# Optimization experiments

Measured on AMD Instinct MI355X. Metric: run time of the kernel, lower is better.

## Reference

```python
import jax, jax.numpy as jnp
import numpy as np
from math import sqrt

SIZE = 4096
NR_CORES = 2
RANK = 16
D = 64  # core_size: D**NR_CORES == SIZE


def setup_inputs() -> dict:
    key = jax.random.key(0)
    k_x, k_c0, k_c1, k_b = jax.random.split(key, 4)
    t = 1.0 / sqrt(SIZE)
    sigma = (t * sqrt(RANK) ** (1 - NR_CORES)) ** (1.0 / NR_CORES)
    x = jax.random.normal(k_x, (2, 4096, SIZE), dtype=jnp.float32)
    core0 = sigma * jax.random.normal(k_c0, (D, D, D, RANK, 1), dtype=jnp.float32)
    core1 = sigma * jax.random.normal(k_c1, (D, D, D, 1, RANK), dtype=jnp.float32)
    bias = sqrt(1.0 / SIZE) * jax.random.uniform(k_b, (SIZE,), minval=-1.0, maxval=1.0, dtype=jnp.float32)
    return {"x": x, "core0": core0, "core1": core1, "bias": bias}


def _btt_forward(x, cores, bias):
    d, c, size = D, NR_CORES, SIZE
    G = cores[0]  # (d,...,d, r, 1)
    for idx, core in enumerate(cores[1:]):
        j = d ** (idx + 1)
        i = d ** (c - idx - 1)
        core_r = core.reshape(j, d, i, core.shape[-2], core.shape[-1])
        G_r = G.reshape(j, d ** (idx + 1), i, G.shape[-2], G.shape[-1])
        # contract rank dim b: (j,x,i,cb) x (j,y,i,ba) -> (j,x,y,i,c,a)
        G = jnp.einsum('jxicb,jyiba->jxyica', core_r, G_r)
    G = G.reshape(size, size)
    out = x.reshape(-1, size) @ G + bias
    return out.reshape(x.shape)


def reference(x, core0, core1, bias):
    return _btt_forward(x, [core0, core1], bias)
```

## Files before the change

### kernel.cpp

```cpp
#include <hip/hip_runtime.h>
#include <hip/hip_bf16.h>
#include <stdint.h>
#include <stddef.h>

using bf16 = __hip_bfloat16;

typedef __attribute__((ext_vector_type(4))) float f32x4;
typedef __attribute__((ext_vector_type(8))) short bf16x8;
typedef __attribute__((ext_vector_type(4))) unsigned short u16x4;

#define K_DIM 4096
#define M_ROWS 8192
#define BM 256
#define BN 256
#define BK 64
#define NT (K_DIM / BK)
#define MT2 (M_ROWS / BM)
#define NT2 (K_DIM / BN)

template<int M> struct MC { static constexpr int value = M; };

__global__ void conv_bf16(const float* __restrict__ in, bf16* __restrict__ outb, int n4) {
  int idx = blockIdx.x * blockDim.x + threadIdx.x;
  int stride = gridDim.x * blockDim.x;
  for (int k = idx; k < n4; k += stride) {
    f32x4 v = ((const f32x4*)in)[k];
    bf16 tmp[4];
    tmp[0] = __float2bfloat16(v.x);
    tmp[1] = __float2bfloat16(v.y);
    tmp[2] = __float2bfloat16(v.z);
    tmp[3] = __float2bfloat16(v.w);
    ((u16x4*)outb)[k] = *(const u16x4*)tmp;
  }
}

__global__ void build_gt(const float* __restrict__ core0, const float* __restrict__ core1,
                         bf16* __restrict__ GT) {
  int j = blockIdx.x >> 6;
  int i = blockIdx.x & 63;
  __shared__ float c0s[64][16];
  __shared__ float c1s[64][16];
  int t = threadIdx.x;
#pragma unroll
  for (int rep = 0; rep < 4; ++rep) {
    int idx = rep * 256 + t;
    int row = idx >> 4;
    int b = idx & 15;
    size_t base = ((size_t)(j * 64 + row) * 64 + i) * 16 + b;
    c1s[row][b] = core1[base];
    c0s[row][b] = core0[base];
  }
  __syncthreads();
  int x = t & 63;
  int ys = t >> 6;
  float r1[16];
#pragma unroll
  for (int b = 0; b < 16; ++b) r1[b] = c1s[x][b];
#pragma unroll
  for (int yy = 0; yy < 16; ++yy) {
    int y = ys * 16 + yy;
    float acc = 0.f;
#pragma unroll
    for (int b = 0; b < 16; ++b) acc += r1[b] * c0s[y][b];
    GT[((size_t)(y * 64 + i) << 12) + (size_t)(j * 64 + x)] = __float2bfloat16(acc);
  }
}

__device__ __forceinline__ void gload_lds16(const bf16* g, bf16* l) {
  __builtin_amdgcn_global_load_lds(
      (const __attribute__((address_space(1))) unsigned int*)(g),
      (__attribute__((address_space(3))) unsigned int*)(l),
      16, 0, 0);
}

template<int MH>
__device__ __forceinline__ void read_a(bf16x8 (&af)[4][2], const bf16* As,
                                       int abase, int swk0, int swk1) {
#pragma unroll
  for (int mi = 0; mi < 4; ++mi) {
    int off = abase + (MH * 4 + mi) * 1024;
    af[mi][0] = *(const bf16x8*)&As[off + swk0];
    af[mi][1] = *(const bf16x8*)&As[off + swk1];
  }
}

template<int NH>
__device__ __forceinline__ void read_b(bf16x8 (&bfr)[4][2], const bf16* Bs,
                                       int bbase, int swk0, int swk1) {
#pragma unroll
  for (int ni = 0; ni < 2; ++ni) {
    int off = bbase + (NH * 2 + ni) * 1024;
    bfr[NH * 2 + ni][0] = *(const bf16x8*)&Bs[off + swk0];
    bfr[NH * 2 + ni][1] = *(const bf16x8*)&Bs[off + swk1];
  }
}

template<int MH, int NH>
__device__ __forceinline__ void mfma_quad(f32x4 (&acc)[8][4], const bf16x8 (&af)[4][2],
                                          const bf16x8 (&bfr)[4][2]) {
#pragma unroll
  for (int mi = 0; mi < 4; ++mi)
#pragma unroll
    for (int ni = 0; ni < 2; ++ni)
#pragma unroll
      for (int kk = 0; kk < 2; ++kk)
        acc[MH * 4 + mi][NH * 2 + ni] = __builtin_amdgcn_mfma_f32_16x16x32_bf16(
            af[mi][kk], bfr[NH * 2 + ni][kk], acc[MH * 4 + mi][NH * 2 + ni], 0, 0, 0);
}

#define BARRIER() __builtin_amdgcn_s_barrier()
#define SP1() __builtin_amdgcn_s_setprio(1)
#define SP0() __builtin_amdgcn_s_setprio(0)
#define VMCNT4() asm volatile("s_waitcnt vmcnt(4)" ::: "memory")
#define VMCNT0() asm volatile("s_waitcnt vmcnt(0)" ::: "memory")

__global__ __launch_bounds__(512, 2)
void gemm_xg(const bf16* __restrict__ Xb, const bf16* __restrict__ GT,
             const float* __restrict__ bias, float* __restrict__ out) {
  __shared__ bf16 As[2][BM * BK];
  __shared__ bf16 Bs[2][BN * BK];

  int bid = blockIdx.x;
  int sb = (bid & 7) * (MT2 * NT2 / 8) + (bid >> 3);
  int bm = sb >> 4;
  int bn = sb & 15;

  int t = threadIdx.x;
  int lane = t & 63;
  int wid = t >> 6;

  int srow = t >> 3;
  int scol = t & 7;
  int sxor = scol ^ (srow & 7);
  const bf16* gA0 = Xb + ((size_t)(bm * BM + srow) * K_DIM) + sxor * 8;
  const bf16* gB0 = GT + ((size_t)(bn * BN + srow) * K_DIM) + sxor * 8;
  int lbase = srow * BK + scol * 8;

  auto sA = [&](int buf, int h, int kt) {
    const bf16* g = gA0 + (size_t)(h * 128) * K_DIM + (size_t)kt * BK;
    bf16* l = &As[buf][h * 128 * BK + lbase];
    gload_lds16(g, l);
    gload_lds16(g + (size_t)64 * K_DIM, l + 64 * BK);
  };
  auto sB = [&](int buf, int h, int kt) {
    const bf16* g = gB0 + (size_t)(h * 128) * K_DIM + (size_t)kt * BK;
    bf16* l = &Bs[buf][h * 128 * BK + lbase];
    gload_lds16(g, l);
    gload_lds16(g + (size_t)64 * K_DIM, l + 64 * BK);
  };

  int wm = wid >> 2;
  int wn = wid & 3;
  int lr = lane & 15;
  int g4 = lane >> 4;
  int x7 = lr & 7;
  int swk0 = ((g4 ^ x7) << 3);
  int swk1 = (((4 + g4) ^ x7) << 3);
  int abase = (wm * 128 + lr) * BK;
  int bbase = (wn * 64 + lr) * BK;

  f32x4 acc[8][4] = {};
  bf16x8 af[4][2];
  bf16x8 bfr[4][2];

  auto tile = [&](int kt, const bf16* Ab, const bf16* Bb, int obuf, int cbuf, auto mode) {
    constexpr int MODE = decltype(mode)::value;
    if (MODE == 2) { VMCNT0(); } else { VMCNT4(); }
    BARRIER();
    if (MODE < 2) { sA(obuf, 0, kt + 1); sA(obuf, 1, kt + 1); }
    read_a<0>(af, Ab, abase, swk0, swk1);
    read_b<0>(bfr, Bb, bbase, swk0, swk1);
    read_b<1>(bfr, Bb, bbase, swk0, swk1);
    SP1();
    mfma_quad<0, 0>(acc, af, bfr);
    mfma_quad<0, 1>(acc, af, bfr);
    SP0();
    read_a<1>(af, Ab, abase, swk0, swk1);
    SP1();
    mfma_quad<1, 0>(acc, af, bfr);
    mfma_quad<1, 1>(acc, af, bfr);
    SP0();
    BARRIER();
    if (MODE == 0) { sB(cbuf, 0, kt + 2); sB(cbuf, 1, kt + 2); }
  };

  const bf16* A0 = &As[0][0];
  const bf16* B0 = &Bs[0][0];
  const bf16* A1 = &As[1][0];
  const bf16* B1 = &Bs[1][0];

  sB(0, 0, 0); sB(0, 1, 0);
  sA(0, 0, 0); sA(0, 1, 0);
  sB(1, 0, 1); sB(1, 1, 1);

#pragma unroll 1
  for (int i = 0; i < NT / 2 - 1; ++i) {
    tile(2 * i,     A0, B0, 1, 0, MC<0>{});
    tile(2 * i + 1, A1, B1, 0, 1, MC<0>{});
  }
  tile(NT - 2, A0, B0, 1, 0, MC<1>{});
  tile(NT - 1, A1, B1, 0, 1, MC<2>{});

  int colbase = bn * BN + wn * 64 + lr;
  int rowbase = bm * BM + wm * 128 + g4 * 4;
#pragma unroll
  for (int ni = 0; ni < 4; ++ni) {
    int col = colbase + ni * 16;
    float bv = bias[col];
#pragma unroll
    for (int mi = 0; mi < 8; ++mi) {
#pragma unroll
      for (int r = 0; r < 4; ++r) {
        int row = rowbase + mi * 16 + r;
        out[(size_t)row * K_DIM + col] = acc[mi][ni][r] + bv;
      }
    }
  }
}

extern "C" void kernel_launch(void* const* d_in, const int* in_sizes, int n_in,
                              void* d_out, int out_size, void* d_ws, size_t ws_size,
                              hipStream_t stream) {
  const float* x     = (const float*)d_in[0];
  const float* core0 = (const float*)d_in[1];
  const float* core1 = (const float*)d_in[2];
  const float* bias  = (const float*)d_in[3];
  float* out = (float*)d_out;

  bf16* Xb = (bf16*)d_ws;
  bf16* GT = (bf16*)((char*)d_ws + (size_t)M_ROWS * K_DIM * sizeof(bf16));

  conv_bf16<<<2048, 256, 0, stream>>>(x, Xb, (M_ROWS * K_DIM) / 4);
  build_gt<<<4096, 256, 0, stream>>>(core0, core1, GT);
  gemm_xg<<<MT2 * NT2, 512, 0, stream>>>(Xb, GT, bias, out);
}
```

Before: 297.4 us.

## Restructure GEMM main loop into ping-pong phases overlapping LDS reads with MFMA

The bf16 GEMM main loop becomes a multi-phase schedule. Each tile is split into four barrier-separated phases. The MFMAs for the second M-half of the previous tile are deferred into the next tile's first phase, and partial lgkmcnt waits with sched_barriers let LDS fragment reads and global-to-LDS prefetches overlap compute. The intent is to hide LDS read latency and balance issue across waves. It adds more barriers and more live fragment registers, which may hurt occupancy at 2 blocks per CU or add sync overhead.

```diff
diff --git a/kernel.cpp b/kernel.cpp
--- a/kernel.cpp
+++ b/kernel.cpp
@@ -73,42 +73,15 @@
       16, 0, 0);
 }
 
-template<int MH>
-__device__ __forceinline__ void read_a(bf16x8 (&af)[4][2], const bf16* As,
-                                       int abase, int swk0, int swk1) {
-#pragma unroll
-  for (int mi = 0; mi < 4; ++mi) {
-    int off = abase + (MH * 4 + mi) * 1024;
-    af[mi][0] = *(const bf16x8*)&As[off + swk0];
-    af[mi][1] = *(const bf16x8*)&As[off + swk1];
-  }
-}
-
-template<int NH>
-__device__ __forceinline__ void read_b(bf16x8 (&bfr)[4][2], const bf16* Bs,
-                                       int bbase, int swk0, int swk1) {
-#pragma unroll
-  for (int ni = 0; ni < 2; ++ni) {
-    int off = bbase + (NH * 2 + ni) * 1024;
-    bfr[NH * 2 + ni][0] = *(const bf16x8*)&Bs[off + swk0];
-    bfr[NH * 2 + ni][1] = *(const bf16x8*)&Bs[off + swk1];
-  }
-}
-
-template<int MH, int NH>
-__device__ __forceinline__ void mfma_quad(f32x4 (&acc)[8][4], const bf16x8 (&af)[4][2],
-                                          const bf16x8 (&bfr)[4][2]) {
-#pragma unroll
-  for (int mi = 0; mi < 4; ++mi)
-#pragma unroll
-    for (int ni = 0; ni < 2; ++ni)
-#pragma unroll
-      for (int kk = 0; kk < 2; ++kk)
-        acc[MH * 4 + mi][NH * 2 + ni] = __builtin_amdgcn_mfma_f32_16x16x32_bf16(
-            af[mi][kk], bfr[NH * 2 + ni][kk], acc[MH * 4 + mi][NH * 2 + ni], 0, 0, 0);
-}
-
-#define BARRIER() __builtin_amdgcn_s_barrier()
+#define BARRIER() asm volatile("s_barrier" ::: "memory")
+#define LGKM8F() do { \
+    asm volatile("s_waitcnt lgkmcnt(8)" ::: "memory"); \
+    __builtin_amdgcn_sched_barrier(0); \
+  } while (0)
+#define LGKM0F() do { \
+    asm volatile("s_waitcnt lgkmcnt(0)" ::: "memory"); \
+    __builtin_amdgcn_sched_barrier(0); \
+  } while (0)
 #define SP1() __builtin_amdgcn_s_setprio(1)
 #define SP0() __builtin_amdgcn_s_setprio(0)
 #define VMCNT4() asm volatile("s_waitcnt vmcnt(4)" ::: "memory")
@@ -160,46 +133,106 @@
   int bbase = (wn * 64 + lr) * BK;
 
   f32x4 acc[8][4] = {};
-  bf16x8 af[4][2];
-  bf16x8 bfr[4][2];
-
-  auto tile = [&](int kt, const bf16* Ab, const bf16* Bb, int obuf, int cbuf, auto mode) {
-    constexpr int MODE = decltype(mode)::value;
-    if (MODE == 2) { VMCNT0(); } else { VMCNT4(); }
-    BARRIER();
-    if (MODE < 2) { sA(obuf, 0, kt + 1); sA(obuf, 1, kt + 1); }
-    read_a<0>(af, Ab, abase, swk0, swk1);
-    read_b<0>(bfr, Bb, bbase, swk0, swk1);
-    read_b<1>(bfr, Bb, bbase, swk0, swk1);
-    SP1();
-    mfma_quad<0, 0>(acc, af, bfr);
-    mfma_quad<0, 1>(acc, af, bfr);
-    SP0();
-    read_a<1>(af, Ab, abase, swk0, swk1);
-    SP1();
-    mfma_quad<1, 0>(acc, af, bfr);
-    mfma_quad<1, 1>(acc, af, bfr);
-    SP0();
-    BARRIER();
-    if (MODE == 0) { sB(cbuf, 0, kt + 2); sB(cbuf, 1, kt + 2); }
-  };
-
-  const bf16* A0 = &As[0][0];
-  const bf16* B0 = &Bs[0][0];
-  const bf16* A1 = &As[1][0];
-  const bf16* B1 = &Bs[1][0];
+  bf16x8 a0[4][2], a1[4][2];
+  bf16x8 b0[2][2], b1[2][2];
+
+  auto rdA0 = [&](const bf16* Ab) {
+#pragma unroll
+    for (int mi = 0; mi < 4; ++mi) {
+      int off = abase + mi * 1024;
+      a0[mi][0] = *(const bf16x8*)&Ab[off + swk0];
+      a0[mi][1] = *(const bf16x8*)&Ab[off + swk1];
+    }
+  };
+  auto rdA1 = [&](const bf16* Ab) {
+#pragma unroll
+    for (int mi = 0; mi < 4; ++mi) {
+      int off = abase + (4 + mi) * 1024;
+      a1[mi][0] = *(const bf16x8*)&Ab[off + swk0];
+      a1[mi][1] = *(const bf16x8*)&Ab[off + swk1];
+    }
+  };
+  auto rdB01 = [&](const bf16* Bb) {
+#pragma unroll
+    for (int ni = 0; ni < 2; ++ni) {
+      int off = bbase + ni * 1024;
+      b0[ni][0] = *(const bf16x8*)&Bb[off + swk0];
+      b0[ni][1] = *(const bf16x8*)&Bb[off + swk1];
+    }
+#pragma unroll
+    for (int ni = 0; ni < 2; ++ni) {
+      int off = bbase + (2 + ni) * 1024;
+      b1[ni][0] = *(const bf16x8*)&Bb[off + swk0];
+      b1[ni][1] = *(const bf16x8*)&Bb[off + swk1];
+    }
+  };
+  auto MQ = [&](int mh, int nh, bf16x8 (&av)[4][2], bf16x8 (&bv)[2][2]) {
+#pragma unroll
+    for (int mi = 0; mi < 4; ++mi)
+#pragma unroll
+      for (int ni = 0; ni < 2; ++ni)
+#pragma unroll
+        for (int kk = 0; kk < 2; ++kk)
+          acc[mh * 4 + mi][nh * 2 + ni] = __builtin_amdgcn_mfma_f32_16x16x32_bf16(
+              av[mi][kk], bv[ni][kk], acc[mh * 4 + mi][nh * 2 + ni], 0, 0, 0);
+  };
+
+  const bf16* A0p = &As[0][0];
+  const bf16* B0p = &Bs[0][0];
+  const bf16* A1p = &As[1][0];
+  const bf16* B1p = &Bs[1][0];
+
+  auto tile = [&](int kt, const bf16* Ac, const bf16* Bc, int c, int nb, auto modec) {
+    constexpr int MODE = decltype(modec)::value;
+    constexpr bool PREV = (MODE != 0);
+    constexpr bool SB = (MODE <= 1);
+    constexpr bool SA = (MODE <= 2);
+
+    if (SA) sA(nb, 0, kt + 1);
+    rdA0(Ac);
+    BARRIER();
+    LGKM8F();
+    if (PREV) { SP1(); MQ(1, 0, a1, b0); MQ(1, 1, a1, b1); SP0(); }
+    BARRIER();
+
+    if (SA) sA(nb, 1, kt + 1);
+    rdB01(Bc);
+    BARRIER();
+
+    if (SB) sB(c, 0, kt + 2);
+    rdA1(Ac);
+    BARRIER();
+    LGKM8F();
+    SP1(); MQ(0, 0, a0, b0); SP0();
+    BARRIER();
+
+    if (SB) sB(c, 1, kt + 2);
+    if (MODE <= 1)      { VMCNT4(); }
+    else if (MODE == 2) { VMCNT0(); }
+    BARRIER();
+    LGKM8F();
+    SP1(); MQ(0, 1, a0, b1); SP0();
+    BARRIER();
+  };
 
   sB(0, 0, 0); sB(0, 1, 0);
   sA(0, 0, 0); sA(0, 1, 0);
   sB(1, 0, 1); sB(1, 1, 1);
-
+  VMCNT4();
+  BARRIER();
+
+  tile(0, A0p, B0p, 0, 1, MC<0>{});
+  tile(1, A1p, B1p, 1, 0, MC<1>{});
 #pragma unroll 1
-  for (int i = 0; i < NT / 2 - 1; ++i) {
-    tile(2 * i,     A0, B0, 1, 0, MC<0>{});
-    tile(2 * i + 1, A1, B1, 0, 1, MC<0>{});
-  }
-  tile(NT - 2, A0, B0, 1, 0, MC<1>{});
-  tile(NT - 1, A1, B1, 0, 1, MC<2>{});
+  for (int i = 1; i < NT / 2 - 1; ++i) {
+    tile(2 * i,     A0p, B0p, 0, 1, MC<1>{});
+    tile(2 * i + 1, A1p, B1p, 1, 0, MC<1>{});
+  }
+  tile(NT - 2, A0p, B0p, 0, 1, MC<2>{});
+  tile(NT - 1, A1p, B1p, 1, 0, MC<3>{});
+
+  LGKM0F();
+  SP1(); MQ(1, 0, a1, b0); MQ(1, 1, a1, b1); SP0();
 
   int colbase = bn * BN + wn * 64 + lr;
   int rowbase = bm * BM + wm * 128 + g4 * 4;
```

New measurement: 365.6 us. 22.9% more time.
